# Kernel tuning notes

Hardware: AMD Instinct MI355X
Metric: run time of the kernel (lower is better)

## Reference

```python
import math
import jax, jax.numpy as jnp
import numpy as np

R = 4  # upsample_factor
C_FEAT = 22
FEAT_SLICES = {4: (0, 9), 6: (9, 22)}
SH_SLICES = {0: (0, 1), 2: (1, 6)}
AGG_PATHS = [(4, 0, 4), (4, 2, 4), (4, 2, 6), (6, 0, 6), (6, 2, 4), (6, 2, 6)]
TP_PATHS = [(4, 4, 4), (4, 4, 6), (4, 6, 4), (4, 6, 6), (6, 4, 4), (6, 4, 6), (6, 6, 4), (6, 6, 6)]
AGG_NPATH = {4: 3, 6: 3}
TP_NPATH = {4: 4, 6: 4}


def _cg(j1, m1, j2, m2, j3, m3):
    # Condon-Shortley Clebsch-Gordan <j1 m1 j2 m2 | j3 m3> (Racah formula)
    if m1 + m2 != m3:
        return 0.0
    f = math.factorial
    pre = (2 * j3 + 1) * f(j1 + j2 - j3) * f(j1 - j2 + j3) * f(-j1 + j2 + j3) / f(j1 + j2 + j3 + 1)
    pre *= f(j1 + m1) * f(j1 - m1) * f(j2 + m2) * f(j2 - m2) * f(j3 + m3) * f(j3 - m3)
    kmin = max(0, j2 - j3 - m1, j1 - j3 + m2)
    kmax = min(j1 + j2 - j3, j1 - m1, j2 + m2)
    s = 0.0
    for k in range(kmin, kmax + 1):
        s += (-1) ** k / (f(k) * f(j1 + j2 - j3 - k) * f(j1 - m1 - k) * f(j2 + m2 - k) * f(j3 - j2 + m1 + k) * f(j3 - j1 - m2 + k))
    return math.sqrt(pre) * s


def _q(l):
    # change of basis real SH -> complex SH (rows: real m, cols: complex m), with (-i)^l phase
    q = np.zeros((2 * l + 1, 2 * l + 1), dtype=np.complex128)
    q[l, l] = 1.0
    s2 = 1.0 / math.sqrt(2.0)
    for m in range(1, l + 1):
        q[l + m, l + m] = (-1) ** m * s2
        q[l + m, l - m] = s2
        q[l - m, l - m] = 1j * s2
        q[l - m, l + m] = -1j * (-1) ** m * s2
    return ((-1j) ** l) * q


def _w3j_real(l1, l2, l3):
    # Wigner 3j tensor in the real spherical-harmonic basis (invariant, unit Frobenius norm)
    w = np.zeros((2 * l1 + 1, 2 * l2 + 1, 2 * l3 + 1))
    for m1 in range(-l1, l1 + 1):
        for m2 in range(-l2, l2 + 1):
            m3 = -(m1 + m2)
            if abs(m3) <= l3:
                w[l1 + m1, l2 + m2, l3 + m3] = ((-1) ** (l1 - l2 - m3)) / math.sqrt(2 * l3 + 1) * _cg(l1, m1, l2, m2, l3, -m3)
    c = np.einsum('ai,bj,ck,ijk->abc', _q(l1), _q(l2), _q(l3), w.astype(np.complex128))
    return np.real(c).astype(np.float32)  # l1+l2+l3 even -> real


CG = {p: jnp.asarray(_w3j_real(*p)) for p in set(AGG_PATHS) | set(TP_PATHS)}


def _sh_kernel():
    # even-l real SH (integral normalization) at the 4 fixed 2x2 kernel directions
    s = 1.0 / math.sqrt(2.0)
    dirs = np.array([[-s, -s, 0.0], [s, -s, 0.0], [-s, s, 0.0], [s, s, 0.0]])
    x, y, z = dirs[:, 0], dirs[:, 1], dirs[:, 2]
    c2 = math.sqrt(15.0 / math.pi)
    sh = np.stack([
        np.full(4, 0.5 / math.sqrt(math.pi)),      # l=0
        0.5 * c2 * x * y,                           # l=2, m=-2
        0.5 * c2 * y * z,                           # l=2, m=-1
        0.25 * math.sqrt(5.0 / math.pi) * (3 * z ** 2 - 1.0),  # l=2, m=0
        0.5 * c2 * x * z,                           # l=2, m=1
        0.25 * c2 * (x ** 2 - y ** 2),              # l=2, m=2
    ], axis=1)
    return jnp.asarray(sh.astype(np.float32))  # (4, 6)


SH_KERNEL = _sh_kernel()


def setup_inputs() -> dict:
    key = jax.random.key(0)
    k1, k2, k3, k4 = jax.random.split(key, 4)
    H = W = 256
    return {
        'f4': jax.random.normal(k1, (H * W, 9), dtype=jnp.float32),
        'f6': jax.random.normal(k2, (H * W, 13), dtype=jnp.float32),
        'img_h': H,
        'img_w': W,
        'w_agg': jax.random.normal(k3, (6,), dtype=jnp.float32) * 0.1,
        'w_tp': jax.random.normal(k4, (8,), dtype=jnp.float32) * 0.1,
    }


def reference(f4, f6, img_h, img_w, w_agg, w_tp):
    H, W = int(img_h), int(img_w)
    Hr, Wr = H * R, W * R
    N = Hr * Wr
    # 1. nearest-neighbour upsample of concatenated irreps (H,W,22) -> (Hr,Wr,22)
    feat = jnp.concatenate([f4, f6], axis=-1).reshape(H, W, C_FEAT)
    feat_hr = jnp.repeat(jnp.repeat(feat, R, axis=0), R, axis=1)
    # 2. gather 2x2 patches with replicate padding (matches unfold k ordering (dh,dw))
    pad = jnp.pad(feat_hr, ((0, 1), (0, 1), (0, 0)), mode='edge')
    patches = jnp.stack([pad[dh:dh + Hr, dw:dw + Wr] for dh, dw in ((0, 0), (0, 1), (1, 0), (1, 1))], axis=2)
    patches = patches.reshape(N, 4, C_FEAT)  # (N,4,22)
    # tp_aggregate(neighbour, sh) summed over the 4 neighbours -> context (N,22)
    context = jnp.zeros((N, C_FEAT), dtype=feat.dtype)
    for i, (l1, l2, l3) in enumerate(AGG_PATHS):
        a0, a1 = FEAT_SLICES[l1]
        b0, b1 = SH_SLICES[l2]
        c0, c1 = FEAT_SLICES[l3]
        alpha = math.sqrt((2 * l3 + 1) / AGG_NPATH[l3])
        contrib = jnp.einsum('nka,kb,abc->nc', patches[:, :, a0:a1], SH_KERNEL[:, b0:b1], CG[(l1, l2, l3)])
        context = context.at[:, c0:c1].add((w_agg[i] * alpha) * contrib)
    # 3. tp(feat_self, context)
    feat_flat = feat_hr.reshape(N, C_FEAT)
    out = jnp.zeros((N, C_FEAT), dtype=feat.dtype)
    for i, (l1, l2, l3) in enumerate(TP_PATHS):
        a0, a1 = FEAT_SLICES[l1]
        b0, b1 = FEAT_SLICES[l2]
        c0, c1 = FEAT_SLICES[l3]
        alpha = math.sqrt((2 * l3 + 1) / TP_NPATH[l3])
        contrib = jnp.einsum('na,nb,abc->nc', feat_flat[:, a0:a1], context[:, b0:b1], CG[(l1, l2, l3)])
        out = out.at[:, c0:c1].add((w_tp[i] * alpha) * contrib)
    # 4. residual from the NN-upsampled features
    f4_out = out[:, :9] + feat_flat[:, :9]
    f6_out = out[:, 9:] + feat_flat[:, 9:]
    return f4_out, f6_out, (Hr, Wr)
```

## Files before the change

kernel.cpp:

```cpp
#include <hip/hip_runtime.h>
#include <hip/hip_bf16.h>
#include <math.h>

typedef __attribute__((ext_vector_type(8))) short short8;
typedef __attribute__((ext_vector_type(4))) float f32x4;
typedef __attribute__((ext_vector_type(2))) float f32x2;
typedef __attribute__((ext_vector_type(4))) unsigned int u32x4;
typedef __attribute__((ext_vector_type(2))) unsigned int u32x2;
typedef __attribute__((ext_vector_type(2))) long long2v;

__constant__ float c_fact[20] = {
    1.0f, 1.0f, 2.0f, 6.0f, 24.0f, 120.0f, 720.0f, 5040.0f, 40320.0f, 362880.0f,
    3628800.0f, 39916800.0f, 479001600.0f, 6227020800.0f, 87178291200.0f,
    1307674368000.0f, 20922789888000.0f, 355687428096000.0f,
    6402373705728000.0f, 121645100408832000.0f};
__constant__ float c_invf[20] = {
    1.0f, 1.0f, 0.5f, 0.16666666666666666f, 0.041666666666666664f,
    0.008333333333333333f, 0.001388888888888889f, 1.984126984126984e-4f,
    2.48015873015873e-5f, 2.755731922398589e-6f, 2.755731922398589e-7f,
    2.505210838544172e-8f, 2.08767569878681e-9f, 1.6059043836821613e-10f,
    1.1470745597729725e-11f, 7.647163731819816e-13f, 4.779477332387385e-14f,
    2.8114572543455206e-15f, 1.5619206968586225e-16f, 8.22063524662433e-18f};

__device__ float cgd(int j1, int m1, int j2, int m2, int j3, int m3) {
  if (m1 + m2 != m3) return 0.0f;
  float pre = (float)(2 * j3 + 1) * c_fact[j1 + j2 - j3] * c_fact[j1 - j2 + j3] *
              c_fact[-j1 + j2 + j3] * c_invf[j1 + j2 + j3 + 1];
  pre *= c_fact[j1 + m1] * c_fact[j1 - m1] * c_fact[j2 + m2] * c_fact[j2 - m2] *
         c_fact[j3 + m3] * c_fact[j3 - m3];
  int kmin = max(0, max(j2 - j3 - m1, j1 - j3 + m2));
  int kmax = min(j1 + j2 - j3, min(j1 - m1, j2 + m2));
  float s = 0.0f;
  for (int k = kmin; k <= kmax; ++k) {
    float d = c_invf[k] * c_invf[j1 + j2 - j3 - k] * c_invf[j1 - m1 - k] *
              c_invf[j2 + m2 - k] * c_invf[j3 - j2 + m1 + k] * c_invf[j3 - j1 - m2 + k];
    s += ((k & 1) ? -d : d);
  }
  return sqrtf(pre) * s;
}

__device__ float wstd(int l1, int l2, int l3, int i, int j, int k) {
  int m1 = i - l1, m2 = j - l2, m3 = k - l3;
  if (m1 + m2 + m3 != 0) return 0.0f;
  int e = l1 - l2 - m3;
  float sgn = (e & 1) ? -1.0f : 1.0f;
  return sgn * (1.0f / sqrtf((float)(2 * l3 + 1))) * cgd(l1, m1, l2, m2, l3, -m3);
}

__device__ int qrow(int l, int a, int idx[2], float vr[2], float vi[2]) {
  const float s2 = 0.70710678118654752440f;
  int m = a - l;
  if (m == 0) { idx[0] = l; vr[0] = 1.0f; vi[0] = 0.0f; return 1; }
  if (m > 0) {
    idx[0] = l + m; vr[0] = (m & 1) ? -s2 : s2; vi[0] = 0.0f;
    idx[1] = l - m; vr[1] = s2;                 vi[1] = 0.0f;
    return 2;
  }
  int mm = -m;
  idx[0] = l - mm; vr[0] = 0.0f; vi[0] = s2;
  idx[1] = l + mm; vr[1] = 0.0f; vi[1] = (mm & 1) ? s2 : -s2;
  return 2;
}

__device__ float w3j_real(int l1, int l2, int l3, int a, int b, int c) {
  int i1[2], i2[2], i3[2];
  float r1[2], s1[2], r2[2], s2v[2], r3[2], s3[2];
  int n1 = qrow(l1, a, i1, r1, s1);
  int n2 = qrow(l2, b, i2, r2, s2v);
  int n3 = qrow(l3, c, i3, r3, s3);
  float re = 0.0f;
  for (int x = 0; x < n1; ++x)
    for (int y = 0; y < n2; ++y)
      for (int z = 0; z < n3; ++z) {
        float w = wstd(l1, l2, l3, i1[x], i2[y], i3[z]);
        if (w == 0.0f) continue;
        float pr = r1[x] * r2[y] - s1[x] * s2v[y];
        float pi = r1[x] * s2v[y] + s1[x] * r2[y];
        float qr = pr * r3[z] - pi * s3[z];
        re += qr * w;
      }
  int L = l1 + l2 + l3;
  return ((L & 3) == 0) ? re : -re;
}

__device__ float sh_val(int k, int col) {
  const float PI_ = 3.14159265358979323846f;
  float sgn = (k == 0 || k == 3) ? 1.0f : -1.0f;
  if (col == 0) return 0.5f / sqrtf(PI_);
  if (col == 1) return sgn * 0.25f * sqrtf(15.0f / PI_);
  if (col == 3) return -0.25f * sqrtf(5.0f / PI_);
  return 0.0f;
}

__device__ __forceinline__ unsigned short bf16u(float x) {
  __hip_bfloat16 h = __float2bfloat16(x);
  return __builtin_bit_cast(unsigned short, h);
}
__device__ __forceinline__ float b2f(unsigned short u) {
  unsigned int v = ((unsigned int)u) << 16;
  return __builtin_bit_cast(float, v);
}

__global__ void eq_setup(const float* __restrict__ w_agg, const float* __restrict__ w_tp,
                         const int* __restrict__ ph, const int* __restrict__ pw,
                         float* __restrict__ out, long long tail_off,
                         unsigned short* __restrict__ ws) {
  int gid = blockIdx.x * 256 + threadIdx.x;
  if (gid == 0) {
    out[tail_off]     = (float)(ph[0] * 4);
    out[tail_off + 1] = (float)(pw[0] * 4);
  }
  if (gid < 22528) {
    int a = gid >> 10;
    int rem = gid & 1023;
    int nt = rem >> 9;
    int l = (rem >> 3) & 63;
    int e = rem & 7;
    int b = ((l >> 4) << 3) + e;
    int c = nt * 16 + (l & 15);
    float v = 0.f;
    if (b < 22 && c < 22) {
      int l1 = (a < 9) ? 4 : 6, l2 = (b < 9) ? 4 : 6, l3 = (c < 9) ? 4 : 6;
      int a_ = (a < 9) ? a : a - 9, b_ = (b < 9) ? b : b - 9, c_ = (c < 9) ? c : c - 9;
      int idx = ((l1 == 6) ? 4 : 0) + ((l2 == 6) ? 2 : 0) + ((l3 == 6) ? 1 : 0);
      float alpha = sqrtf((float)(2 * l3 + 1) * 0.25f);
      v = w_tp[idx] * alpha * w3j_real(l1, l2, l3, a_, b_, c_);
    }
    int pk = __builtin_amdgcn_cvt_pk_fp8_f32(v, 0.f, 0, 0);
    int nidx = ((a >> 1) << 11) + l * 32 + ((((a & 1) << 1) | nt) << 3) + e;
    ((unsigned char*)ws)[nidx] = (unsigned char)(pk & 0xff);
  } else if (gid < 26624) {
    int s = gid - 22528;
    int km = s >> 10;
    int rem = s & 1023;
    int nt = rem >> 9;
    int l = (rem >> 3) & 63;
    int e = rem & 7;
    int a = ((l >> 4) << 3) + e;
    int c = nt * 16 + (l & 15);
    float v = 0.f;
    if (a < 22 && c < 22) {
      int l1 = (a < 9) ? 4 : 6, l3 = (c < 9) ? 4 : 6;
      int a_ = (a < 9) ? a : a - 9, c_ = (c < 9) ? c : c - 9;
      float acc = 0.0f;
      float alpha = sqrtf((float)(2 * l3 + 1) / 3.0f);
      if (l1 == l3) {
        int i = (l1 == 4) ? 0 : 3;
        acc += w_agg[i] * alpha * sh_val(km, 0) * w3j_real(l1, 0, l3, a_, 0, c_);
      }
      {
        int i = (l1 == 4) ? ((l3 == 4) ? 1 : 2) : ((l3 == 4) ? 4 : 5);
        float t = 0.0f;
        for (int bb = 0; bb < 5; ++bb) {
          float shv = sh_val(km, 1 + bb);
          if (shv != 0.0f) t += shv * w3j_real(l1, 2, l3, a_, bb, c_);
        }
        acc += w_agg[i] * alpha * t;
      }
      v = acc;
    }
    ws[11264 + s] = bf16u(v);
  }
}

__device__ __forceinline__ void load_lds16(const unsigned int* g, unsigned int* l) {
  __builtin_amdgcn_global_load_lds(
      (const __attribute__((address_space(1))) unsigned int*)g,
      (__attribute__((address_space(3))) unsigned int*)l, 16, 0, 0);
}

#define WAVE_LDS_FENCE() do { \
    asm volatile("s_waitcnt lgkmcnt(0)" ::: "memory"); \
    __builtin_amdgcn_sched_barrier(0); } while (0)

__global__ __launch_bounds__(512, 6) void eq_main(
    const float* __restrict__ f4, const float* __restrict__ f6,
    const int* __restrict__ ph, const int* __restrict__ pw,
    const unsigned short* __restrict__ ws, float* __restrict__ out) {
  const int H = ph[0], Wc = pw[0];
  const int bx = (Wc + 31) >> 5;
  const long long ntiles = (long long)bx * H;
  const int Wr = Wc << 2;
  const long long Npix = (long long)H * Wc * 16;
  float* out6 = out + Npix * 9;

  __shared__ __align__(16) unsigned short LDS[23040];

  const int tid = threadIdx.x;
  const int wv = tid >> 6;
  const int l = tid & 63;
  const long long t = blockIdx.x;
  if (t >= ntiles) return;

  const int y0 = (int)(t / bx);
  const int x0 = (int)(t - (long long)y0 * bx) << 5;
  const int cw0 = x0 + (wv << 2);
  const int SLOT = 11264 + wv * 1472;

  {
    const unsigned int* src = (const unsigned int*)ws;
    unsigned int* dst = (unsigned int*)LDS;
#pragma unroll
    for (int i = 0; i < 3; ++i) {
      int chunk = i * 8 + wv;
      if (chunk < 22) load_lds16(src + chunk * 256 + l * 4, dst + chunk * 256);
    }
  }

  short8 mb[8];
  {
    const unsigned short* msrc = ws + 11264;
#pragma unroll
    for (int i = 0; i < 8; ++i) mb[i] = *(const short8*)(msrc + i * 512 + l * 8);
  }

#pragma unroll
  for (int k = 0; k < 2; ++k) {
    int e = k * 64 + l;
    if (e < 110) {
      int px = e / 11, pr = e - px * 11;
      int dyR = px / 5, col = px - dyR * 5;
      int yy = min(y0 + dyR, H - 1);
      int xx = min(cw0 + col, Wc - 1);
      long long p = (long long)yy * Wc + xx;
      int ca = 2 * pr;
      float v0 = (ca < 9) ? f4[p * 9 + ca] : f6[p * 13 + ca - 9];
      float v1 = (ca + 1 < 9) ? f4[p * 9 + ca + 1] : f6[p * 13 + ca - 8];
      unsigned int pk = (unsigned int)bf16u(v0) | ((unsigned int)bf16u(v1) << 16);
      *(unsigned int*)&LDS[SLOT + px * 24 + ca] = pk;
    } else if (e < 120) {
      *(unsigned int*)&LDS[SLOT + (e - 110) * 24 + 22] = 0u;
    }
  }
  WAVE_LDS_FENCE();

  const int l15 = l & 15;
  const int lg = l >> 4;
  const int q = l15 & 3;
  const int lcell = l15 >> 2;
  const int a0 = lg << 3;

  f32x4 c0 = {0.f, 0.f, 0.f, 0.f}, c1 = {0.f, 0.f, 0.f, 0.f};
#pragma unroll
  for (int km = 0; km < 4; ++km) {
    short8 av = (short8)0;
    if (a0 < 24) {
      int dy = (km >> 1) & (q >> 1);
      int dx = km & q & 1;
      av = *(const short8*)&LDS[SLOT + (dy * 5 + lcell + dx) * 24 + a0];
    }
    c0 = __builtin_amdgcn_mfma_f32_16x16x32_bf16(av, mb[2 * km], c0, 0, 0, 0);
    c1 = __builtin_amdgcn_mfma_f32_16x16x32_bf16(av, mb[2 * km + 1], c1, 0, 0, 0);
  }

  unsigned int fvp[11];
  {
    const unsigned int* fp = (const unsigned int*)&LDS[SLOT + lcell * 24];
    u32x4 q0 = *(const u32x4*)fp;
    u32x4 q1 = *(const u32x4*)(fp + 4);
    u32x2 q2 = *(const u32x2*)(fp + 8);
    unsigned int q3 = fp[10];
#pragma unroll
    for (int j = 0; j < 4; ++j) { fvp[j] = q0[j]; fvp[4 + j] = q1[j]; }
    fvp[8] = q2[0]; fvp[9] = q2[1]; fvp[10] = q3;
  }
  const float r4 = b2f(LDS[SLOT + lg * 24 + l15]);
  const float r6 = (l15 < 6) ? b2f(LDS[SLOT + lg * 24 + 16 + l15]) : 0.f;

  float* ctxf = (float*)&LDS[SLOT + 256];
  {
    *(f32x4*)(ctxf + l15 * 24 + (lg << 2)) = c0;
    if (lg == 0) {
      *(f32x4*)(ctxf + l15 * 24 + 16) = c1;
    } else if (lg == 1) {
      f32x4 tail = {c1[0], c1[1], 0.f, 0.f};
      *(f32x4*)(ctxf + l15 * 24 + 20) = tail;
    }
  }
  WAVE_LDS_FENCE();

  f32x2 cv2[4];
  {
    f32x4 lo = {0.f, 0.f, 0.f, 0.f}, hi = {0.f, 0.f, 0.f, 0.f};
    if (a0 < 24) {
      lo = *(const f32x4*)(ctxf + l15 * 24 + a0);
      hi = *(const f32x4*)(ctxf + l15 * 24 + a0 + 4);
    }
    cv2[0][0] = lo[0]; cv2[0][1] = lo[1];
    cv2[1][0] = lo[2]; cv2[1][1] = lo[3];
    cv2[2][0] = hi[0]; cv2[2][1] = hi[1];
    cv2[3][0] = hi[2]; cv2[3][1] = hi[3];
  }

  __syncthreads();

  f32x4 oE0 = {0.f, 0.f, 0.f, 0.f}, oE1 = {0.f, 0.f, 0.f, 0.f};
  f32x4 oO0 = {0.f, 0.f, 0.f, 0.f}, oO1 = {0.f, 0.f, 0.f, 0.f};
  const char* Wb = (const char*)LDS;
#pragma unroll
  for (int ap = 0; ap < 11; ++ap) {
    const float sE = __builtin_bit_cast(float, fvp[ap] << 16);
    const float sO = __builtin_bit_cast(float, fvp[ap] & 0xffff0000u);
    const long2v wE = *(const long2v*)(Wb + ap * 2048 + l * 32);
    const long2v wO = *(const long2v*)(Wb + ap * 2048 + l * 32 + 16);
    {
      const f32x2 s2 = {sE, sE};
      f32x2 p0 = cv2[0] * s2, p1 = cv2[1] * s2, p2 = cv2[2] * s2, p3 = cv2[3] * s2;
      int lo = __builtin_amdgcn_cvt_pk_fp8_f32(p0[0], p0[1], 0, 0);
      lo = __builtin_amdgcn_cvt_pk_fp8_f32(p1[0], p1[1], lo, 1);
      int hi = __builtin_amdgcn_cvt_pk_fp8_f32(p2[0], p2[1], 0, 0);
      hi = __builtin_amdgcn_cvt_pk_fp8_f32(p3[0], p3[1], hi, 1);
      long av = (long)(((unsigned long long)(unsigned int)hi << 32) | (unsigned int)lo);
      oE0 = __builtin_amdgcn_mfma_f32_16x16x32_fp8_fp8(av, wE[0], oE0, 0, 0, 0);
      oE1 = __builtin_amdgcn_mfma_f32_16x16x32_fp8_fp8(av, wE[1], oE1, 0, 0, 0);
    }
    {
      const f32x2 s2 = {sO, sO};
      f32x2 p0 = cv2[0] * s2, p1 = cv2[1] * s2, p2 = cv2[2] * s2, p3 = cv2[3] * s2;
      int lo = __builtin_amdgcn_cvt_pk_fp8_f32(p0[0], p0[1], 0, 0);
      lo = __builtin_amdgcn_cvt_pk_fp8_f32(p1[0], p1[1], lo, 1);
      int hi = __builtin_amdgcn_cvt_pk_fp8_f32(p2[0], p2[1], 0, 0);
      hi = __builtin_amdgcn_cvt_pk_fp8_f32(p3[0], p3[1], hi, 1);
      long av = (long)(((unsigned long long)(unsigned int)hi << 32) | (unsigned int)lo);
      oO0 = __builtin_amdgcn_mfma_f32_16x16x32_fp8_fp8(av, wO[0], oO0, 0, 0, 0);
      oO1 = __builtin_amdgcn_mfma_f32_16x16x32_fp8_fp8(av, wO[1], oO1, 0, 0, 0);
    }
  }
  WAVE_LDS_FENCE();

  float* px4 = (float*)&LDS[SLOT];
  float* px6 = px4 + 288;
#pragma unroll
  for (int r = 0; r < 4; ++r) {
    const float v  = oE0[r] + oO0[r] + r4;
    const float v1 = oE1[r] + oO1[r] + r6;
    const int qy = r >> 1;
    float* p4 = px4 + qy * 144;
    float* p6 = px6 + qy * 208;
    if (r & 1) {
      const int px = (lg << 2) + 3;
      if (l15 < 9) p4[px * 9 + l15] = v; else p6[px * 13 + l15 - 9] = v;
      if (l15 < 6) p6[px * 13 + 7 + l15] = v1;
    } else {
#pragma unroll
      for (int dx = 0; dx < 3; ++dx) {
        const int px = (lg << 2) + dx;
        if (l15 < 9) p4[px * 9 + l15] = v; else p6[px * 13 + l15 - 9] = v;
        if (l15 < 6) p6[px * 13 + 7 + l15] = v1;
      }
    }
  }
  WAVE_LDS_FENCE();

  const long long y4 = (long long)(y0 << 2);
  if (cw0 + 4 <= Wc) {
#pragma unroll
    for (int ry = 0; ry < 4; ++ry) {
      const int qy = (ry == 3) ? 1 : 0;
      float* o4p = out + ((y4 + ry) * Wr + (cw0 << 2)) * 9;
      float* o6p = out6 + ((y4 + ry) * Wr + (cw0 << 2)) * 13;
      if (l < 36) *(f32x4*)(o4p + (l << 2)) = *(const f32x4*)(px4 + qy * 144 + (l << 2));
      if (l < 52) *(f32x4*)(o6p + (l << 2)) = *(const f32x4*)(px6 + qy * 208 + (l << 2));
    }
  } else {
    const int px = l & 15;
    const int ry = l >> 4;
    const int qy = (ry == 3) ? 1 : 0;
    const int hrx = (cw0 << 2) + px;
    if (hrx < Wr) {
      const long long rowb = (y4 + ry) * Wr + hrx;
      float* o4 = out + rowb * 9;
      float* o6 = out6 + rowb * 13;
#pragma unroll
      for (int ch = 0; ch < 9; ++ch) o4[ch] = px4[qy * 144 + px * 9 + ch];
#pragma unroll
      for (int ch = 0; ch < 13; ++ch) o6[ch] = px6[qy * 208 + px * 13 + ch];
    }
  }
}

extern "C" void kernel_launch(void* const* d_in, const int* in_sizes, int n_in,
                              void* d_out, int out_size, void* d_ws, size_t ws_size,
                              hipStream_t stream) {
  const float* f4 = (const float*)d_in[0];
  const float* f6 = (const float*)d_in[1];
  const int* ph = (const int*)d_in[2];
  const int* pw = (const int*)d_in[3];
  const float* wagg = (const float*)d_in[4];
  const float* wtp = (const float*)d_in[5];
  float* out = (float*)d_out;
  unsigned short* wsu = (unsigned short*)d_ws;

  long long HW = (long long)in_sizes[0] / 9;
  long long tail = (long long)out_size - 2;

  eq_setup<<<104, 256, 0, stream>>>(wagg, wtp, ph, pw, out, tail, wsu);

  int S = (int)(sqrt((double)HW) + 0.5);
  long long nb;
  if ((long long)S * S == HW) {
    nb = (long long)((S + 31) / 32) * S;
  } else {
    nb = HW;
  }
  eq_main<<<(int)nb, 512, 0, stream>>>(f4, f6, ph, pw, wsu, out);
}
```

Before: 46.56 us.

## Process two tiles per block and prefetch second tile's inputs during first

```diff
diff --git a/kernel.cpp b/kernel.cpp
--- a/kernel.cpp
+++ b/kernel.cpp
@@ -173,73 +173,10 @@
     asm volatile("s_waitcnt lgkmcnt(0)" ::: "memory"); \
     __builtin_amdgcn_sched_barrier(0); } while (0)
 
-__global__ __launch_bounds__(512, 6) void eq_main(
-    const float* __restrict__ f4, const float* __restrict__ f6,
-    const int* __restrict__ ph, const int* __restrict__ pw,
-    const unsigned short* __restrict__ ws, float* __restrict__ out) {
-  const int H = ph[0], Wc = pw[0];
-  const int bx = (Wc + 31) >> 5;
-  const long long ntiles = (long long)bx * H;
-  const int Wr = Wc << 2;
-  const long long Npix = (long long)H * Wc * 16;
-  float* out6 = out + Npix * 9;
-
-  __shared__ __align__(16) unsigned short LDS[23040];
-
-  const int tid = threadIdx.x;
-  const int wv = tid >> 6;
-  const int l = tid & 63;
-  const long long t = blockIdx.x;
-  if (t >= ntiles) return;
-
-  const int y0 = (int)(t / bx);
-  const int x0 = (int)(t - (long long)y0 * bx) << 5;
-  const int cw0 = x0 + (wv << 2);
-  const int SLOT = 11264 + wv * 1472;
-
-  {
-    const unsigned int* src = (const unsigned int*)ws;
-    unsigned int* dst = (unsigned int*)LDS;
-#pragma unroll
-    for (int i = 0; i < 3; ++i) {
-      int chunk = i * 8 + wv;
-      if (chunk < 22) load_lds16(src + chunk * 256 + l * 4, dst + chunk * 256);
-    }
-  }
-
-  short8 mb[8];
-  {
-    const unsigned short* msrc = ws + 11264;
-#pragma unroll
-    for (int i = 0; i < 8; ++i) mb[i] = *(const short8*)(msrc + i * 512 + l * 8);
-  }
-
-#pragma unroll
-  for (int k = 0; k < 2; ++k) {
-    int e = k * 64 + l;
-    if (e < 110) {
-      int px = e / 11, pr = e - px * 11;
-      int dyR = px / 5, col = px - dyR * 5;
-      int yy = min(y0 + dyR, H - 1);
-      int xx = min(cw0 + col, Wc - 1);
-      long long p = (long long)yy * Wc + xx;
-      int ca = 2 * pr;
-      float v0 = (ca < 9) ? f4[p * 9 + ca] : f6[p * 13 + ca - 9];
-      float v1 = (ca + 1 < 9) ? f4[p * 9 + ca + 1] : f6[p * 13 + ca - 8];
-      unsigned int pk = (unsigned int)bf16u(v0) | ((unsigned int)bf16u(v1) << 16);
-      *(unsigned int*)&LDS[SLOT + px * 24 + ca] = pk;
-    } else if (e < 120) {
-      *(unsigned int*)&LDS[SLOT + (e - 110) * 24 + 22] = 0u;
-    }
-  }
-  WAVE_LDS_FENCE();
-
-  const int l15 = l & 15;
-  const int lg = l >> 4;
-  const int q = l15 & 3;
-  const int lcell = l15 >> 2;
-  const int a0 = lg << 3;
-
+__device__ __forceinline__ void k1_and_ctx(
+    unsigned short* LDS, int SLOT, const short8* mb,
+    int l15, int lg, int q, int lcell, int a0,
+    unsigned int* fvp, float& r4, float& r6, f32x2* cv2) {
   f32x4 c0 = {0.f, 0.f, 0.f, 0.f}, c1 = {0.f, 0.f, 0.f, 0.f};
 #pragma unroll
   for (int km = 0; km < 4; ++km) {
@@ -252,8 +189,6 @@
     c0 = __builtin_amdgcn_mfma_f32_16x16x32_bf16(av, mb[2 * km], c0, 0, 0, 0);
     c1 = __builtin_amdgcn_mfma_f32_16x16x32_bf16(av, mb[2 * km + 1], c1, 0, 0, 0);
   }
-
-  unsigned int fvp[11];
   {
     const unsigned int* fp = (const unsigned int*)&LDS[SLOT + lcell * 24];
     u32x4 q0 = *(const u32x4*)fp;
@@ -264,9 +199,8 @@
     for (int j = 0; j < 4; ++j) { fvp[j] = q0[j]; fvp[4 + j] = q1[j]; }
     fvp[8] = q2[0]; fvp[9] = q2[1]; fvp[10] = q3;
   }
-  const float r4 = b2f(LDS[SLOT + lg * 24 + l15]);
-  const float r6 = (l15 < 6) ? b2f(LDS[SLOT + lg * 24 + 16 + l15]) : 0.f;
-
+  r4 = b2f(LDS[SLOT + lg * 24 + l15]);
+  r6 = (l15 < 6) ? b2f(LDS[SLOT + lg * 24 + 16 + l15]) : 0.f;
   float* ctxf = (float*)&LDS[SLOT + 256];
   {
     *(f32x4*)(ctxf + l15 * 24 + (lg << 2)) = c0;
@@ -278,8 +212,6 @@
     }
   }
   WAVE_LDS_FENCE();
-
-  f32x2 cv2[4];
   {
     f32x4 lo = {0.f, 0.f, 0.f, 0.f}, hi = {0.f, 0.f, 0.f, 0.f};
     if (a0 < 24) {
@@ -291,11 +223,11 @@
     cv2[2][0] = hi[0]; cv2[2][1] = hi[1];
     cv2[3][0] = hi[2]; cv2[3][1] = hi[3];
   }
-
-  __syncthreads();
-
-  f32x4 oE0 = {0.f, 0.f, 0.f, 0.f}, oE1 = {0.f, 0.f, 0.f, 0.f};
-  f32x4 oO0 = {0.f, 0.f, 0.f, 0.f}, oO1 = {0.f, 0.f, 0.f, 0.f};
+}
+
+__device__ __forceinline__ void k2_compute(
+    const unsigned short* LDS, int l, const unsigned int* fvp, const f32x2* cv2,
+    f32x4& oE0, f32x4& oE1, f32x4& oO0, f32x4& oO1) {
   const char* Wb = (const char*)LDS;
 #pragma unroll
   for (int ap = 0; ap < 11; ++ap) {
@@ -326,8 +258,13 @@
       oO1 = __builtin_amdgcn_mfma_f32_16x16x32_fp8_fp8(av, wO[1], oO1, 0, 0, 0);
     }
   }
-  WAVE_LDS_FENCE();
-
+}
+
+__device__ __forceinline__ void epilogue_and_write(
+    unsigned short* LDS, int SLOT, int l, int l15, int lg,
+    const f32x4& oE0, const f32x4& oE1, const f32x4& oO0, const f32x4& oO1,
+    float r4, float r6, int y0, int cw0, int Wc, int Wr,
+    float* out, float* out6) {
   float* px4 = (float*)&LDS[SLOT];
   float* px6 = px4 + 288;
 #pragma unroll
@@ -351,7 +288,6 @@
     }
   }
   WAVE_LDS_FENCE();
-
   const long long y4 = (long long)(y0 << 2);
   if (cw0 + 4 <= Wc) {
 #pragma unroll
@@ -376,6 +312,141 @@
 #pragma unroll
       for (int ch = 0; ch < 13; ++ch) o6[ch] = px6[qy * 208 + px * 13 + ch];
     }
+  }
+}
+
+__global__ __launch_bounds__(512, 6) void eq_main(
+    const float* __restrict__ f4, const float* __restrict__ f6,
+    const int* __restrict__ ph, const int* __restrict__ pw,
+    const unsigned short* __restrict__ ws, float* __restrict__ out) {
+  const int H = ph[0], Wc = pw[0];
+  const int bx = (Wc + 31) >> 5;
+  const long long ntiles = (long long)bx * H;
+  const int Wr = Wc << 2;
+  const long long Npix = (long long)H * Wc * 16;
+  float* out6 = out + Npix * 9;
+
+  __shared__ __align__(16) unsigned short LDS[23040];
+
+  const int tid = threadIdx.x;
+  const int wv = tid >> 6;
+  const int l = tid & 63;
+  const long long t0 = (long long)blockIdx.x * 2;
+  if (t0 >= ntiles) return;
+  const bool t1ok = (t0 + 1) < ntiles;
+
+  const int y0a = (int)(t0 / bx);
+  const int cw0a = (((int)(t0 - (long long)y0a * bx)) << 5) + (wv << 2);
+  int y0b = 0, cw0b = 0;
+  if (t1ok) {
+    const long long t1 = t0 + 1;
+    y0b = (int)(t1 / bx);
+    cw0b = (((int)(t1 - (long long)y0b * bx)) << 5) + (wv << 2);
+  }
+  const int SLOT = 11264 + wv * 1472;
+
+  {
+    const unsigned int* src = (const unsigned int*)ws;
+    unsigned int* dst = (unsigned int*)LDS;
+#pragma unroll
+    for (int i = 0; i < 3; ++i) {
+      int chunk = i * 8 + wv;
+      if (chunk < 22) load_lds16(src + chunk * 256 + l * 4, dst + chunk * 256);
+    }
+  }
+  short8 mb[8];
+  {
+    const unsigned short* msrc = ws + 11264;
+#pragma unroll
+    for (int i = 0; i < 8; ++i) mb[i] = *(const short8*)(msrc + i * 512 + l * 8);
+  }
+#pragma unroll
+  for (int k = 0; k < 2; ++k) {
+    int e = k * 64 + l;
+    if (e < 110) {
+      int px = e / 11, pr = e - px * 11;
+      int dyR = px / 5, col = px - dyR * 5;
+      int yy = min(y0a + dyR, H - 1);
+      int xx = min(cw0a + col, Wc - 1);
+      long long p = (long long)yy * Wc + xx;
+      int ca = 2 * pr;
+      float v0 = (ca < 9) ? f4[p * 9 + ca] : f6[p * 13 + ca - 9];
+      float v1 = (ca + 1 < 9) ? f4[p * 9 + ca + 1] : f6[p * 13 + ca - 8];
+      unsigned int pk = (unsigned int)bf16u(v0) | ((unsigned int)bf16u(v1) << 16);
+      *(unsigned int*)&LDS[SLOT + px * 24 + ca] = pk;
+    } else if (e < 120) {
+      *(unsigned int*)&LDS[SLOT + (e - 110) * 24 + 22] = 0u;
+    }
+  }
+  WAVE_LDS_FENCE();
+
+  const int l15 = l & 15;
+  const int lg = l >> 4;
+  const int q = l15 & 3;
+  const int lcell = l15 >> 2;
+  const int a0 = lg << 3;
+
+  unsigned int fvp[11];
+  float r4, r6;
+  f32x2 cv2[4];
+  k1_and_ctx(LDS, SLOT, mb, l15, lg, q, lcell, a0, fvp, r4, r6, cv2);
+
+  __syncthreads();
+
+  float pf0 = 0.f, pf1 = 0.f, pf2 = 0.f, pf3 = 0.f;
+  if (t1ok) {
+#pragma unroll
+    for (int k = 0; k < 2; ++k) {
+      int e = k * 64 + l;
+      if (e < 110) {
+        int px = e / 11, pr = e - px * 11;
+        int dyR = px / 5, col = px - dyR * 5;
+        int yy = min(y0b + dyR, H - 1);
+        int xx = min(cw0b + col, Wc - 1);
+        long long p = (long long)yy * Wc + xx;
+        int ca = 2 * pr;
+        float v0 = (ca < 9) ? f4[p * 9 + ca] : f6[p * 13 + ca - 9];
+        float v1 = (ca + 1 < 9) ? f4[p * 9 + ca + 1] : f6[p * 13 + ca - 8];
+        if (k == 0) { pf0 = v0; pf1 = v1; } else { pf2 = v0; pf3 = v1; }
+      }
+    }
+  }
+
+  {
+    f32x4 oE0 = {0.f, 0.f, 0.f, 0.f}, oE1 = {0.f, 0.f, 0.f, 0.f};
+    f32x4 oO0 = {0.f, 0.f, 0.f, 0.f}, oO1 = {0.f, 0.f, 0.f, 0.f};
+    k2_compute(LDS, l, fvp, cv2, oE0, oE1, oO0, oO1);
+    WAVE_LDS_FENCE();
+    epilogue_and_write(LDS, SLOT, l, l15, lg, oE0, oE1, oO0, oO1,
+                       r4, r6, y0a, cw0a, Wc, Wr, out, out6);
+  }
+  if (!t1ok) return;
+
+  WAVE_LDS_FENCE();
+
+#pragma unroll
+  for (int k = 0; k < 2; ++k) {
+    int e = k * 64 + l;
+    if (e < 110) {
+      int px = e / 11, pr = e - px * 11;
+      float v0 = (k == 0) ? pf0 : pf2;
+      float v1 = (k == 0) ? pf1 : pf3;
+      unsigned int pk = (unsigned int)bf16u(v0) | ((unsigned int)bf16u(v1) << 16);
+      *(unsigned int*)&LDS[SLOT + px * 24 + 2 * pr] = pk;
+    } else if (e < 120) {
+      *(unsigned int*)&LDS[SLOT + (e - 110) * 24 + 22] = 0u;
+    }
+  }
+  WAVE_LDS_FENCE();
+
+  k1_and_ctx(LDS, SLOT, mb, l15, lg, q, lcell, a0, fvp, r4, r6, cv2);
+  {
+    f32x4 oE0 = {0.f, 0.f, 0.f, 0.f}, oE1 = {0.f, 0.f, 0.f, 0.f};
+    f32x4 oO0 = {0.f, 0.f, 0.f, 0.f}, oO1 = {0.f, 0.f, 0.f, 0.f};
+    k2_compute(LDS, l, fvp, cv2, oE0, oE1, oO0, oO1);
+    WAVE_LDS_FENCE();
+    epilogue_and_write(LDS, SLOT, l, l15, lg, oE0, oE1, oO0, oO1,
+                       r4, r6, y0b, cw0b, Wc, Wr, out, out6);
   }
 }
 
@@ -399,9 +470,10 @@
   int S = (int)(sqrt((double)HW) + 0.5);
   long long nb;
   if ((long long)S * S == HW) {
-    nb = (long long)((S + 31) / 32) * S;
+    long long nt = (long long)((S + 31) / 32) * S;
+    nb = (nt + 1) / 2;
   } else {
-    nb = HW;
+    nb = HW / 2 + 2;
   }
   eq_main<<<(int)nb, 512, 0, stream>>>(f4, f6, ph, pw, wsu, out);
 }
```

After: 60.40 us. 29.7% more time.
